# Kernel tuning notes

Measured on AMD Instinct MI355X. Metric: run time of the kernel, lower is better.

The kernel has to match this reference:

```python
import jax, jax.numpy as jnp
import numpy as np

# MSDeformAttn-style fusion config (canonical deformable-DETR defaults)
D = 256      # d_model
NH = 8       # n_heads
NP = 4       # n_points per level
NL = 2       # n_levels (= num_feature_levels: modality v and modality i)
B, H, W = 4, 64, 64


def setup_inputs() -> dict:
    key = jax.random.key(0)
    ks = jax.random.split(key, 8)
    s = 0.02
    return {
        'input_v': jax.random.normal(ks[0], (B, D, H, W), jnp.float32),
        'input_i': jax.random.normal(ks[1], (B, D, H, W), jnp.float32),
        'W_value': jax.random.normal(ks[2], (D, D), jnp.float32) * s,
        'b_value': jnp.zeros((D,), jnp.float32),
        'W_off':   jax.random.normal(ks[3], (D, NH * NL * NP * 2), jnp.float32) * s,
        'b_off':   jax.random.normal(ks[4], (NH * NL * NP * 2,), jnp.float32) * s,
        'W_attn':  jax.random.normal(ks[5], (D, NH * NL * NP), jnp.float32) * s,
        'b_attn':  jnp.zeros((NH * NL * NP,), jnp.float32),
        'W_out':   jax.random.normal(ks[6], (D, D), jnp.float32) * s,
        'b_out':   jnp.zeros((D,), jnp.float32),
    }


def _bilinear_sample(value_l, locs, Hl, Wl):
    # value_l: (B, NH, HW, dh)  flattened per-level value
    # locs:    (B, Lq, NH, NP, 2) normalized sampling locations in [0,1]
    # returns  (B, NH, Lq, NP, dh); grid_sample semantics: zeros padding, align_corners=False
    b, nh, hw, dh = value_l.shape
    lq = locs.shape[1]
    x = locs[..., 0] * Wl - 0.5
    y = locs[..., 1] * Hl - 0.5
    x0 = jnp.floor(x)
    y0 = jnp.floor(y)
    dx = x - x0
    dy = y - y0
    x0i = x0.astype(jnp.int32)
    y0i = y0.astype(jnp.int32)
    out = jnp.zeros((b, nh, lq, NP, dh), value_l.dtype)
    corners = [
        (x0i,     y0i,     (1 - dx) * (1 - dy)),
        (x0i + 1, y0i,     dx * (1 - dy)),
        (x0i,     y0i + 1, (1 - dx) * dy),
        (x0i + 1, y0i + 1, dx * dy),
    ]
    for xi, yi, wgt in corners:
        valid = ((xi >= 0) & (xi < Wl) & (yi >= 0) & (yi < Hl)).astype(value_l.dtype)
        idx = jnp.clip(yi, 0, Hl - 1) * Wl + jnp.clip(xi, 0, Wl - 1)      # (B,Lq,NH,NP)
        idx_t = idx.transpose(0, 2, 1, 3).reshape(b, nh, lq * NP, 1)       # (B,NH,Lq*NP,1)
        g = jnp.take_along_axis(value_l, idx_t, axis=2)                    # (B,NH,Lq*NP,dh)
        g = g.reshape(b, nh, lq, NP, dh)
        w_t = (wgt * valid).transpose(0, 2, 1, 3)[..., None]               # (B,NH,Lq,NP,1)
        out = out + g * w_t
    return out


def reference(input_v, input_i, W_value, b_value, W_off, b_off, W_attn, b_attn, W_out, b_out):
    b, c, h, w = input_v.shape
    hw = h * w
    lq = NL * hw
    dh = c // NH

    # flatten both modalities into one token sequence (level 0 = v, level 1 = i)
    src_v = input_v.reshape(b, c, hw).transpose(0, 2, 1)
    src_i = input_i.reshape(b, c, hw).transpose(0, 2, 1)
    src = jnp.concatenate([src_v, src_i], axis=1)                          # (B, Lq, C)

    value = (src @ W_value + b_value).reshape(b, lq, NH, dh)
    value = value.transpose(0, 2, 1, 3)                                    # (B, NH, Lq, dh)
    value_levels = [value[:, :, :hw], value[:, :, hw:]]

    offsets = (src @ W_off + b_off).reshape(b, lq, NH, NL, NP, 2)
    attn = jax.nn.softmax((src @ W_attn + b_attn).reshape(b, lq, NH, NL * NP), axis=-1)
    attn = attn.reshape(b, lq, NH, NL, NP)

    # reference points: normalized pixel centers, same grid for both levels
    xs = (jnp.arange(w, dtype=jnp.float32) + 0.5) / w
    ys = (jnp.arange(h, dtype=jnp.float32) + 0.5) / h
    gy, gx = jnp.meshgrid(ys, xs, indexing='ij')
    ref = jnp.stack([gx.reshape(-1), gy.reshape(-1)], axis=-1)             # (HW, 2)
    ref = jnp.concatenate([ref, ref], axis=0)                              # (Lq, 2)

    norm = jnp.array([w, h], dtype=jnp.float32)
    locs = ref[None, :, None, None, None, :] + offsets / norm              # (B,Lq,NH,NL,NP,2)

    sampled = jnp.stack(
        [_bilinear_sample(value_levels[l], locs[:, :, :, l], h, w) for l in range(NL)],
        axis=3)                                                            # (B,NH,Lq,NL,NP,dh)

    fused = jnp.einsum('bqhlp,bhqlpd->bqhd', attn, sampled).reshape(b, lq, c)
    out = fused @ W_out + b_out                                            # (B, Lq, C)

    out_v = out[:, :hw]
    out_i = out[:, hw:]
    o = out_v + out_i                                                      # (B, HW, C)
    return o.transpose(0, 2, 1).reshape(b, c, h, w)
```

## Files before the change

### kernel.cpp

```cpp
#include <hip/hip_runtime.h>

#define HW 4096
#define LQ 8192
#define DD 256

typedef __bf16 bf16x8 __attribute__((ext_vector_type(8)));
typedef float  f32x4  __attribute__((ext_vector_type(4)));
typedef float  f32x2  __attribute__((ext_vector_type(2)));
typedef unsigned int u32;
typedef u32 u32x4 __attribute__((ext_vector_type(4)));
typedef u32 u32x2 __attribute__((ext_vector_type(2)));

__device__ __forceinline__ float bflo(u32 u) { return __uint_as_float(u << 16); }
__device__ __forceinline__ float bfhi(u32 u) { return __uint_as_float(u & 0xffff0000u); }

#define GLOAD16(g, l) __builtin_amdgcn_global_load_lds(                     \
    (__attribute__((address_space(1))) void*)(g),                          \
    (__attribute__((address_space(3))) void*)(l), 16, 0, 0)

__global__ __launch_bounds__(256) void prep_all(const float* __restrict__ in_v,
                                                const float* __restrict__ in_i,
                                                const float* __restrict__ Wv,
                                                const float* __restrict__ Wo,
                                                const float* __restrict__ Wa,
                                                const float* __restrict__ Wout,
                                                char* __restrict__ srcS,
                                                char* __restrict__ WcatT,
                                                char* __restrict__ WoutT)
{
    __shared__ float tile[64][68];
    if (blockIdx.z < 8) {
        const int q0 = blockIdx.x * 64;
        const int k0 = blockIdx.y * 64;
        const int bz = blockIdx.z;
        const float* src = ((bz & 1) ? in_i : in_v) + (size_t)(bz >> 1) * (DD * HW);
        const int t  = threadIdx.x;
        const int ql = (t & 15) * 4;
        const int kl = t >> 4;
#pragma unroll
        for (int rr = 0; rr < 4; ++rr) {
            const float4 v = *(const float4*)(src + (size_t)(k0 + kl + rr * 16) * HW + q0 + ql);
            *(float4*)&tile[kl + rr * 16][ql] = v;
        }
        __syncthreads();
        const int qrow = t >> 2;
        const int kc   = (t & 3) * 16;
        const int row  = (bz >> 1) * LQ + (bz & 1) * HW + q0 + qrow;
        bf16x8 p0, p1;
#pragma unroll
        for (int j = 0; j < 8; ++j) {
            p0[j] = (__bf16)tile[kc + j][qrow];
            p1[j] = (__bf16)tile[kc + 8 + j][qrow];
        }
        char* drow = srcS + (size_t)row * 512;
        const int sw   = (row & 7) << 4;
        const int base = k0 * 2 + kc * 2;
        *(bf16x8*)(drow + ((base)      ^ sw)) = p0;
        *(bf16x8*)(drow + ((base + 16) ^ sw)) = p1;
    } else {
        const int flat = blockIdx.y * 64 + blockIdx.x;
        if (flat >= 120) return;
        const int gi = flat * 256 + threadIdx.x;
        if (gi < 448 * 32) {
            const int row = gi >> 5;
            const int g   = gi & 31;
            const int k   = g * 8;
            const float* col; int stride;
            if (row < 256)      { col = Wv + row;         stride = 256; }
            else if (row < 384) { col = Wo + (row - 256); stride = 128; }
            else                { col = Wa + (row - 384); stride = 64;  }
            bf16x8 p;
#pragma unroll
            for (int j = 0; j < 8; ++j) p[j] = (__bf16)col[(size_t)(k + j) * stride];
            char* d = WcatT + (size_t)row * 512;
            *(bf16x8*)(d + ((g * 16) ^ ((row & 7) << 4))) = p;
        } else {
            const int gj = gi - 448 * 32;
            if (gj >= 256 * 64) return;
            const int c = gj >> 6;
            const int g = gj & 63;
            const int k = (g * 8) & 255;
            bf16x8 p;
#pragma unroll
            for (int j = 0; j < 8; ++j) p[j] = (__bf16)Wout[(size_t)(k + j) * 256 + c];
            char* d = WoutT + (size_t)c * 1024;
            *(bf16x8*)(d + ((g * 16) ^ ((c & 7) << 4))) = p;
        }
    }
}

template<int BN>
__device__ __forceinline__ void proj_tile(char* smem,
                                          const char* __restrict__ srcS,
                                          const char* __restrict__ WcatT,
                                          const float* __restrict__ b_value,
                                          const float* __restrict__ b_off,
                                          const float* __restrict__ b_attn,
                                          __bf16* __restrict__ valueB,
                                          __bf16* __restrict__ offB,
                                          __bf16* __restrict__ attnB,
                                          int M0, int N0)
{
    constexpr int NI = BN / 32;
    char* As = smem;
    char* Bs = smem + 16384;

    const int t = threadIdx.x;
    const int w = t >> 6;
    const int l = t & 63;
    const int lm = l & 15, lk = l >> 4;
    const int wave_m = (w >> 1) * 64;
    const int wave_n = (w & 1) * (BN / 2);

    f32x4 acc[4][NI] = {};

    const char* Ab = As + (wave_m + lm) * 128;
    const char* Bb = Bs + (wave_n + lm) * 128;
    const int go0 = (lk ^ (l & 7)) * 16;
    const int go1 = go0 ^ 64;

    for (int kt = 0; kt < 4; ++kt) {
        __syncthreads();
        const int kb = kt * 128;
#pragma unroll
        for (int c = 0; c < 4; ++c) {
            const char* g = srcS + (size_t)(M0 + w * 32 + c * 8 + (l >> 3)) * 512 + kb + (l & 7) * 16;
            GLOAD16(g, As + (w * 4 + c) * 1024);
        }
#pragma unroll
        for (int c = 0; c < NI; ++c) {
            const char* g = WcatT + (size_t)(N0 + w * (BN / 4) + c * 8 + (l >> 3)) * 512 + kb + (l & 7) * 16;
            GLOAD16(g, Bs + (w * NI + c) * 1024);
        }
        __syncthreads();

        bf16x8 af[4], bb[NI];
#pragma unroll
        for (int mi = 0; mi < 4; ++mi) af[mi] = *(const bf16x8*)(Ab + mi * 2048 + go0);
#pragma unroll
        for (int ni = 0; ni < NI; ++ni) bb[ni] = *(const bf16x8*)(Bb + ni * 2048 + go0);
#pragma unroll
        for (int mi = 0; mi < 4; ++mi)
#pragma unroll
            for (int ni = 0; ni < NI; ++ni)
                acc[mi][ni] = __builtin_amdgcn_mfma_f32_16x16x32_bf16(af[mi], bb[ni], acc[mi][ni], 0, 0, 0);
#pragma unroll
        for (int mi = 0; mi < 4; ++mi) af[mi] = *(const bf16x8*)(Ab + mi * 2048 + go1);
#pragma unroll
        for (int ni = 0; ni < NI; ++ni) bb[ni] = *(const bf16x8*)(Bb + ni * 2048 + go1);
#pragma unroll
        for (int mi = 0; mi < 4; ++mi)
#pragma unroll
            for (int ni = 0; ni < NI; ++ni)
                acc[mi][ni] = __builtin_amdgcn_mfma_f32_16x16x32_bf16(af[mi], bb[ni], acc[mi][ni], 0, 0, 0);
    }

    __bf16* outp; const float* bias; int ncols, nbase;
    if (N0 < 256)       { outp = valueB; bias = b_value; ncols = 256; nbase = 0;   }
    else if (N0 < 384)  { outp = offB;   bias = b_off;   ncols = 128; nbase = 256; }
    else                { outp = attnB;  bias = b_attn;  ncols = 64;  nbase = 384; }

#pragma unroll
    for (int ni = 0; ni < NI; ++ni) {
        const int cl = N0 + wave_n + ni * 16 + lm - nbase;
        const float bv = bias[cl];
#pragma unroll
        for (int mi = 0; mi < 4; ++mi) {
            const int row = M0 + wave_m + mi * 16 + lk * 4;
#pragma unroll
            for (int r = 0; r < 4; ++r)
                outp[(size_t)(row + r) * ncols + cl] = (__bf16)(acc[mi][ni][r] + bv);
        }
    }
}

__global__ __launch_bounds__(256) void mfma_proj(const char* __restrict__ srcS,
                                                 const char* __restrict__ WcatT,
                                                 const float* __restrict__ b_value,
                                                 const float* __restrict__ b_off,
                                                 const float* __restrict__ b_attn,
                                                 __bf16* __restrict__ valueB,
                                                 __bf16* __restrict__ offB,
                                                 __bf16* __restrict__ attnB)
{
    __shared__ char smem[32768];
    const int M0 = blockIdx.x * 128;
    if (blockIdx.y < 3)
        proj_tile<128>(smem, srcS, WcatT, b_value, b_off, b_attn,
                       valueB, offB, attnB, M0, blockIdx.y * 128);
    else
        proj_tile<64>(smem, srcS, WcatT, b_value, b_off, b_attn,
                      valueB, offB, attnB, M0, 384);
}

__global__ __launch_bounds__(256) void sample_kernel(const char* __restrict__ valueB,
                                                     const char* __restrict__ offB,
                                                     const char* __restrict__ attnB,
                                                     char* __restrict__ fusedS)
{
    __shared__ u32 wlds[4][128][8];
    const int bid0 = blockIdx.x;
    const int bid  = ((bid0 & 7) << 9) | (bid0 >> 3);
    const int w    = threadIdx.x >> 6;
    const int lane = threadIdx.x & 63;
    const int q2   = lane >> 5;
    const int sub  = lane & 31;
    const int head = sub >> 2;
    const int dl   = sub & 3;

    const int px   = bid & 15;
    const int py   = (bid >> 4) & 31;
    const int half = (bid >> 9) & 1;
    const int b    = bid >> 10;
    const int x    = px * 4 + (w & 1) * 2 + q2;
    const int y    = py * 2 + (w >> 1);
    const int row  = b * LQ + half * HW + y * 64 + x;
    const float fx0 = (float)x;
    const float fy0 = (float)y;

    const u32x4 lgp = *(const u32x4*)(attnB + (size_t)row * 128 + head * 16);
    float e8[8];
#pragma unroll
    for (int j = 0; j < 4; ++j) { e8[2 * j] = bflo(lgp[j]); e8[2 * j + 1] = bfhi(lgp[j]); }
    float mx = e8[0];
#pragma unroll
    for (int j = 1; j < 8; ++j) mx = fmaxf(mx, e8[j]);
    const int pt0 = dl * 2;
    const float ex0 = __expf(e8[pt0] - mx);
    const float ex1 = __expf(e8[pt0 + 1] - mx);
    float sp = ex0 + ex1;
    sp += __shfl_xor(sp, 1);
    sp += __shfl_xor(sp, 2);
    const float inv = 1.0f / sp;

    const u32x2 opk = *(const u32x2*)(offB + (size_t)row * 256 + head * 32 + dl * 8);
    u32* slotp = &wlds[w][q2 * 64 + head * 8 + pt0][0];
#pragma unroll
    for (int i = 0; i < 2; ++i) {
        const float ox = bflo(opk[i]);
        const float oy = bfhi(opk[i]);
        const float aw = (i ? ex1 : ex0) * inv;
        const float xx = fx0 + ox;
        const float yy = fy0 + oy;
        const float xf = floorf(xx), yf = floorf(yy);
        const int   xi = (int)xf,   yi = (int)yf;
        const float dx = xx - xf,   dy = yy - yf;
        const bool vx0 = (unsigned)xi       < 64u;
        const bool vx1 = (unsigned)(xi + 1) < 64u;
        const bool vy0 = (unsigned)yi       < 64u;
        const bool vy1 = (unsigned)(yi + 1) < 64u;
        f32x4 W;
        W[0] = (vx0 && vy0) ? aw * (1.f - dx) * (1.f - dy) : 0.f;
        W[1] = (vx1 && vy0) ? aw * dx * (1.f - dy)         : 0.f;
        W[2] = (vx0 && vy1) ? aw * (1.f - dx) * dy         : 0.f;
        W[3] = (vx1 && vy1) ? aw * dx * dy                 : 0.f;
        const int xc0 = min(max(xi, 0), 63);
        const int xc1 = min(max(xi + 1, 0), 63);
        const int yc0 = min(max(yi, 0), 63) << 6;
        const int yc1 = min(max(yi + 1, 0), 63) << 6;
        const int lvl = ((pt0 + i) >> 2) * HW;
        u32x4 S;
        S[0] = (u32)(lvl + yc0 + xc0) << 9; S[1] = (u32)(lvl + yc0 + xc1) << 9;
        S[2] = (u32)(lvl + yc1 + xc0) << 9; S[3] = (u32)(lvl + yc1 + xc1) << 9;
        *(f32x4*)(slotp + i * 8)     = W;
        *(u32x4*)(slotp + i * 8 + 4) = S;
    }

    const int d8 = dl << 3;
    const char* vb = valueB + (((size_t)(b * LQ)) << 9) + head * 64 + d8 * 2;
    const u32* slotb = &wlds[w][q2 * 64 + head * 8][0];
    f32x2 acc2[4] = {};
    __builtin_amdgcn_s_setprio(1);
#pragma unroll
    for (int pt = 0; pt < 8; ++pt) {
        const f32x4 W = *(const f32x4*)(slotb + pt * 8);
        const u32x4 S = *(const u32x4*)(slotb + pt * 8 + 4);
        const u32x4 g00 = *(const u32x4*)(vb + S[0]);
        const u32x4 g10 = *(const u32x4*)(vb + S[1]);
        const u32x4 g01 = *(const u32x4*)(vb + S[2]);
        const u32x4 g11 = *(const u32x4*)(vb + S[3]);
        const f32x2 w0 = {W[0], W[0]};
        const f32x2 w1 = {W[1], W[1]};
        const f32x2 w2 = {W[2], W[2]};
        const f32x2 w3 = {W[3], W[3]};
#pragma unroll
        for (int j = 0; j < 4; ++j) {
            const f32x2 v00 = {bflo(g00[j]), bfhi(g00[j])};
            const f32x2 v10 = {bflo(g10[j]), bfhi(g10[j])};
            const f32x2 v01 = {bflo(g01[j]), bfhi(g01[j])};
            const f32x2 v11 = {bflo(g11[j]), bfhi(g11[j])};
            acc2[j] += w0 * v00 + w1 * v10 + w2 * v01 + w3 * v11;
        }
    }
    __builtin_amdgcn_s_setprio(0);

    bf16x8 ov;
#pragma unroll
    for (int j = 0; j < 4; ++j) {
        ov[2 * j]     = (__bf16)acc2[j][0];
        ov[2 * j + 1] = (__bf16)acc2[j][1];
    }
    const int bo = (head * 64 + d8 * 2) ^ ((row & 7) << 4);
    *(bf16x8*)(fusedS + (size_t)row * 512 + bo) = ov;
}

__global__ __launch_bounds__(256) void mfma_out(const char* __restrict__ fusedS,
                                                const char* __restrict__ WoutT,
                                                const float* __restrict__ b_out,
                                                float* __restrict__ out)
{
    __shared__ char smem[24576];
    char* As = smem;
    char* Bs = smem + 16384;
    float* Tr = (float*)smem;

    const int M0 = blockIdx.x * 128;
    const int N0 = blockIdx.y * 64;
    const int bi = M0 >> 12;
    const int q0 = M0 & 4095;
    const int t = threadIdx.x;
    const int w = t >> 6;
    const int l = t & 63;
    const int lm = l & 15, lk = l >> 4;
    const int wave_m = (w >> 1) * 64;
    const int wave_n = (w & 1) * 32;

    f32x4 acc[4][2] = {};

    const char* Ab = As + (wave_m + lm) * 128;
    const char* Bb = Bs + (wave_n + lm) * 128;
    const int go0 = (lk ^ (l & 7)) * 16;
    const int go1 = go0 ^ 64;

    for (int kt = 0; kt < 8; ++kt) {
        __syncthreads();
        const int half = kt >> 2;
        const int kb   = (kt & 3) * 128;
#pragma unroll
        for (int c = 0; c < 4; ++c) {
            const char* g = fusedS + (size_t)(bi * LQ + half * HW + q0 + w * 32 + c * 8 + (l >> 3)) * 512
                          + kb + (l & 7) * 16;
            GLOAD16(g, As + (w * 4 + c) * 1024);
        }
#pragma unroll
        for (int c = 0; c < 2; ++c) {
            const char* g = WoutT + (size_t)(N0 + w * 16 + c * 8 + (l >> 3)) * 1024 + kt * 128 + (l & 7) * 16;
            GLOAD16(g, Bs + (w * 2 + c) * 1024);
        }
        __syncthreads();

        bf16x8 af[4], bb[2];
#pragma unroll
        for (int mi = 0; mi < 4; ++mi) af[mi] = *(const bf16x8*)(Ab + mi * 2048 + go0);
#pragma unroll
        for (int ni = 0; ni < 2; ++ni) bb[ni] = *(const bf16x8*)(Bb + ni * 2048 + go0);
#pragma unroll
        for (int mi = 0; mi < 4; ++mi)
#pragma unroll
            for (int ni = 0; ni < 2; ++ni)
                acc[mi][ni] = __builtin_amdgcn_mfma_f32_16x16x32_bf16(af[mi], bb[ni], acc[mi][ni], 0, 0, 0);
#pragma unroll
        for (int mi = 0; mi < 4; ++mi) af[mi] = *(const bf16x8*)(Ab + mi * 2048 + go1);
#pragma unroll
        for (int ni = 0; ni < 2; ++ni) bb[ni] = *(const bf16x8*)(Bb + ni * 2048 + go1);
#pragma unroll
        for (int mi = 0; mi < 4; ++mi)
#pragma unroll
            for (int ni = 0; ni < 2; ++ni)
                acc[mi][ni] = __builtin_amdgcn_mfma_f32_16x16x32_bf16(af[mi], bb[ni], acc[mi][ni], 0, 0, 0);
    }

    float bias2[2];
#pragma unroll
    for (int ni = 0; ni < 2; ++ni) bias2[ni] = 2.0f * b_out[N0 + wave_n + ni * 16 + lm];

#pragma unroll
    for (int h = 0; h < 2; ++h) {
        __syncthreads();
        if ((w >> 1) == h) {
#pragma unroll
            for (int mi = 0; mi < 4; ++mi)
#pragma unroll
                for (int ni = 0; ni < 2; ++ni)
#pragma unroll
                    for (int r = 0; r < 4; ++r)
                        Tr[(wave_n + ni * 16 + lm) * 68 + mi * 16 + lk * 4 + r] = acc[mi][ni][r] + bias2[ni];
        }
        __syncthreads();
        const int c  = t >> 2;
        const int qo = (t & 3) * 16;
        float* dst = out + ((size_t)(bi * DD + N0 + c)) * HW + q0 + h * 64 + qo;
        const float* sp = Tr + c * 68 + qo;
#pragma unroll
        for (int j = 0; j < 4; ++j)
            *(f32x4*)(dst + j * 4) = *(const f32x4*)(sp + j * 4);
    }
}

extern "C" void kernel_launch(void* const* d_in, const int* in_sizes, int n_in,
                              void* d_out, int out_size, void* d_ws, size_t ws_size,
                              hipStream_t stream) {
    const float* in_v    = (const float*)d_in[0];
    const float* in_i    = (const float*)d_in[1];
    const float* W_value = (const float*)d_in[2];
    const float* b_value = (const float*)d_in[3];
    const float* W_off   = (const float*)d_in[4];
    const float* b_off   = (const float*)d_in[5];
    const float* W_attn  = (const float*)d_in[6];
    const float* b_attn  = (const float*)d_in[7];
    const float* W_out   = (const float*)d_in[8];
    const float* b_out   = (const float*)d_in[9];
    float* out = (float*)d_out;

    char* ws = (char*)d_ws;
    __bf16* valueB = (__bf16*)(ws);
    __bf16* offB   = (__bf16*)(ws + 16777216);
    __bf16* attnB  = (__bf16*)(ws + 25165824);
    char*   srcS   = ws + 29360128;
    char*   fusedS = ws + 46137344;
    char*   WcatT  = ws + 62914560;
    char*   WoutT  = ws + 63143936;

    prep_all<<<dim3(64, 4, 9), 256, 0, stream>>>(in_v, in_i, W_value, W_off, W_attn, W_out,
                                                 srcS, WcatT, WoutT);
    mfma_proj<<<dim3(256, 4), 256, 0, stream>>>(srcS, WcatT, b_value, b_off, b_attn,
                                                valueB, offB, attnB);
    sample_kernel<<<dim3(4096), 256, 0, stream>>>((const char*)valueB, (const char*)offB,
                                                  (const char*)attnB, fusedS);
    mfma_out<<<dim3(128, 4), 256, 0, stream>>>(fusedS, WoutT, b_out, out);
}
```

Measured before the change: 72.80 us.

## Stage per-block value neighborhood in LDS for bilinear sampling, per level

Each block now copies an 8x5 pixel window (the block's 4x2 query tile plus a one-pixel halo) of the bf16 value tensor into shared memory with global_load_lds, once for each level. Bilinear corner reads that fall inside the window come from LDS, and the rest fall back to global memory through a flag bit in the slot index. The aim is to cut redundant global and L2 gather traffic from neighbouring queries. In exchange the block needs extra LDS, a prefetch of the whole window per level, and several __syncthreads, and the gain depends on how small the offsets are.

```diff
diff --git a/kernel.cpp b/kernel.cpp
--- a/kernel.cpp
+++ b/kernel.cpp
@@ -198,11 +198,14 @@
                                                      const char* __restrict__ attnB,
                                                      char* __restrict__ fusedS)
 {
+    __shared__ char region[20480];
     __shared__ u32 wlds[4][128][8];
+
     const int bid0 = blockIdx.x;
     const int bid  = ((bid0 & 7) << 9) | (bid0 >> 3);
-    const int w    = threadIdx.x >> 6;
-    const int lane = threadIdx.x & 63;
+    const int t    = threadIdx.x;
+    const int w    = t >> 6;
+    const int lane = t & 63;
     const int q2   = lane >> 5;
     const int sub  = lane & 31;
     const int head = sub >> 2;
@@ -212,11 +215,28 @@
     const int py   = (bid >> 4) & 31;
     const int half = (bid >> 9) & 1;
     const int b    = bid >> 10;
-    const int x    = px * 4 + (w & 1) * 2 + q2;
-    const int y    = py * 2 + (w >> 1);
+    const int xp   = px * 4;
+    const int yp   = py * 2;
+    const int x    = xp + (w & 1) * 2 + q2;
+    const int y    = yp + (w >> 1);
     const int row  = b * LQ + half * HW + y * 64 + x;
     const float fx0 = (float)x;
     const float fy0 = (float)y;
+
+    const size_t vbase = ((size_t)(b * LQ)) << 9;
+    {
+        const int bofs = t * 16;
+#pragma unroll
+        for (int i = 0; i < 5; ++i) {
+            const int byte = i * 4096 + bofs;
+            const int slot = byte >> 9;
+            const int inner = byte & 511;
+            const int gy = min(max(yp - 1 + (slot >> 3), 0), 63);
+            const int gx = min(max(xp - 1 + (slot & 7), 0), 63);
+            const char* g = valueB + vbase + (((size_t)(gy * 64 + gx)) << 9) + inner;
+            GLOAD16(g, region + i * 4096 + w * 1024);
+        }
+    }
 
     const u32x4 lgp = *(const u32x4*)(attnB + (size_t)row * 128 + head * 16);
     float e8[8];
@@ -256,29 +276,53 @@
         W[3] = (vx1 && vy1) ? aw * dx * dy                 : 0.f;
         const int xc0 = min(max(xi, 0), 63);
         const int xc1 = min(max(xi + 1, 0), 63);
-        const int yc0 = min(max(yi, 0), 63) << 6;
-        const int yc1 = min(max(yi + 1, 0), 63) << 6;
-        const int lvl = ((pt0 + i) >> 2) * HW;
+        const int yc0 = min(max(yi, 0), 63);
+        const int yc1 = min(max(yi + 1, 0), 63);
+        const int rx0 = xc0 - (xp - 1), rx1 = xc1 - (xp - 1);
+        const int ry0 = yc0 - (yp - 1), ry1 = yc1 - (yp - 1);
+        const bool inr = ((unsigned)rx0 < 8u) && ((unsigned)rx1 < 8u) &&
+                         ((unsigned)ry0 < 5u) && ((unsigned)ry1 < 5u);
         u32x4 S;
-        S[0] = (u32)(lvl + yc0 + xc0) << 9; S[1] = (u32)(lvl + yc0 + xc1) << 9;
-        S[2] = (u32)(lvl + yc1 + xc0) << 9; S[3] = (u32)(lvl + yc1 + xc1) << 9;
+        if (inr) {
+            S[0] = (u32)(((ry0 << 3) + rx0) << 9);
+            S[1] = (u32)(((ry0 << 3) + rx1) << 9);
+            S[2] = (u32)(((ry1 << 3) + rx0) << 9);
+            S[3] = (u32)(((ry1 << 3) + rx1) << 9);
+        } else {
+            const int lvl = ((pt0 + i) >> 2) * HW;
+            S[0] = ((u32)(lvl + yc0 * 64 + xc0) << 9) | 0x80000000u;
+            S[1] = (u32)(lvl + yc0 * 64 + xc1) << 9;
+            S[2] = (u32)(lvl + yc1 * 64 + xc0) << 9;
+            S[3] = (u32)(lvl + yc1 * 64 + xc1) << 9;
+        }
         *(f32x4*)(slotp + i * 8)     = W;
         *(u32x4*)(slotp + i * 8 + 4) = S;
     }
 
-    const int d8 = dl << 3;
-    const char* vb = valueB + (((size_t)(b * LQ)) << 9) + head * 64 + d8 * 2;
+    const int hd = head * 64 + dl * 16;
+    const char* vbl = valueB + vbase + hd;
+    const char* rb  = region + hd;
     const u32* slotb = &wlds[w][q2 * 64 + head * 8][0];
     f32x2 acc2[4] = {};
+
+    __syncthreads();
     __builtin_amdgcn_s_setprio(1);
 #pragma unroll
-    for (int pt = 0; pt < 8; ++pt) {
+    for (int pt = 0; pt < 4; ++pt) {
         const f32x4 W = *(const f32x4*)(slotb + pt * 8);
         const u32x4 S = *(const u32x4*)(slotb + pt * 8 + 4);
-        const u32x4 g00 = *(const u32x4*)(vb + S[0]);
-        const u32x4 g10 = *(const u32x4*)(vb + S[1]);
-        const u32x4 g01 = *(const u32x4*)(vb + S[2]);
-        const u32x4 g11 = *(const u32x4*)(vb + S[3]);
+        u32x4 g00, g10, g01, g11;
+        if (!(S[0] & 0x80000000u)) {
+            g00 = *(const u32x4*)(rb + S[0]);
+            g10 = *(const u32x4*)(rb + S[1]);
+            g01 = *(const u32x4*)(rb + S[2]);
+            g11 = *(const u32x4*)(rb + S[3]);
+        } else {
+            g00 = *(const u32x4*)(vbl + (size_t)(S[0] & 0x7fffffffu));
+            g10 = *(const u32x4*)(vbl + (size_t)S[1]);
+            g01 = *(const u32x4*)(vbl + (size_t)S[2]);
+            g11 = *(const u32x4*)(vbl + (size_t)S[3]);
+        }
         const f32x2 w0 = {W[0], W[0]};
         const f32x2 w1 = {W[1], W[1]};
         const f32x2 w2 = {W[2], W[2]};
@@ -293,6 +337,54 @@
         }
     }
     __builtin_amdgcn_s_setprio(0);
+    __syncthreads();
+
+    {
+        const int bofs = t * 16;
+#pragma unroll
+        for (int i = 0; i < 5; ++i) {
+            const int byte = i * 4096 + bofs;
+            const int slot = byte >> 9;
+            const int inner = byte & 511;
+            const int gy = min(max(yp - 1 + (slot >> 3), 0), 63);
+            const int gx = min(max(xp - 1 + (slot & 7), 0), 63);
+            const char* g = valueB + vbase + (((size_t)(HW + gy * 64 + gx)) << 9) + inner;
+            GLOAD16(g, region + i * 4096 + w * 1024);
+        }
+    }
+    __syncthreads();
+
+    __builtin_amdgcn_s_setprio(1);
+#pragma unroll
+    for (int pt = 4; pt < 8; ++pt) {
+        const f32x4 W = *(const f32x4*)(slotb + pt * 8);
+        const u32x4 S = *(const u32x4*)(slotb + pt * 8 + 4);
+        u32x4 g00, g10, g01, g11;
+        if (!(S[0] & 0x80000000u)) {
+            g00 = *(const u32x4*)(rb + S[0]);
+            g10 = *(const u32x4*)(rb + S[1]);
+            g01 = *(const u32x4*)(rb + S[2]);
+            g11 = *(const u32x4*)(rb + S[3]);
+        } else {
+            g00 = *(const u32x4*)(vbl + (size_t)(S[0] & 0x7fffffffu));
+            g10 = *(const u32x4*)(vbl + (size_t)S[1]);
+            g01 = *(const u32x4*)(vbl + (size_t)S[2]);
+            g11 = *(const u32x4*)(vbl + (size_t)S[3]);
+        }
+        const f32x2 w0 = {W[0], W[0]};
+        const f32x2 w1 = {W[1], W[1]};
+        const f32x2 w2 = {W[2], W[2]};
+        const f32x2 w3 = {W[3], W[3]};
+#pragma unroll
+        for (int j = 0; j < 4; ++j) {
+            const f32x2 v00 = {bflo(g00[j]), bfhi(g00[j])};
+            const f32x2 v10 = {bflo(g10[j]), bfhi(g10[j])};
+            const f32x2 v01 = {bflo(g01[j]), bfhi(g01[j])};
+            const f32x2 v11 = {bflo(g11[j]), bfhi(g11[j])};
+            acc2[j] += w0 * v00 + w1 * v10 + w2 * v01 + w3 * v11;
+        }
+    }
+    __builtin_amdgcn_s_setprio(0);
 
     bf16x8 ov;
 #pragma unroll
@@ -300,6 +392,7 @@
         ov[2 * j]     = (__bf16)acc2[j][0];
         ov[2 * j + 1] = (__bf16)acc2[j][1];
     }
+    const int d8 = dl << 3;
     const int bo = (head * 64 + d8 * 2) ^ ((row & 7) << 4);
     *(bf16x8*)(fusedS + (size_t)row * 512 + bo) = ov;
 }
```

Result: slower. 92.08 us (+26.5%).
